# Kernel optimization log

Measured on AMD Instinct MI355X. Metric: run time of the kernel, lower is better.

## Reference

```python
import jax, jax.numpy as jnp
import numpy as np

NUM_WIRES = 14
LAYERS = 3
PPL = 3
BATCH = 1024
DIM = 2 ** NUM_WIRES


def setup_inputs() -> dict:
    key = jax.random.key(0)
    k1, k2, k3, k4, k5 = jax.random.split(key, 5)
    sr = jax.random.normal(k1, (BATCH, DIM), jnp.float32)
    si = jax.random.normal(k2, (BATCH, DIM), jnp.float32)
    norm = jnp.sqrt(jnp.sum(sr * sr + si * si, axis=1, keepdims=True))
    sr, si = sr / norm, si / norm  # normalized amplitude-encoded states
    weights = jax.random.normal(k3, (LAYERS, PPL, NUM_WIRES), jnp.float32)
    head_w = jax.random.normal(k4, (1, NUM_WIRES), jnp.float32) / np.sqrt(NUM_WIRES)
    head_b = jax.random.normal(k5, (1,), jnp.float32) * 0.01
    return {"state_real": sr, "state_imag": si, "weights": weights,
            "head_w": head_w, "head_b": head_b}


def _apply_ry_all(st, angles):
    # st: (B,)+(2,)*n complex; apply RY(angles[q]) on each wire q (RYs on distinct wires commute)
    half = angles * 0.5
    c, s = jnp.cos(half), jnp.sin(half)
    for q in range(NUM_WIRES):
        ax = 1 + q
        a0 = jnp.take(st, 0, axis=ax)
        a1 = jnp.take(st, 1, axis=ax)
        n0 = c[q] * a0 - s[q] * a1
        n1 = s[q] * a0 + c[q] * a1
        st = jnp.stack([n0, n1], axis=ax)
    return st


def _apply_cnot(st, ctrl, tgt):
    # flip target axis only where control bit == 1
    ctrl_ax, tgt_ax = 1 + ctrl, 1 + tgt
    flipped = jnp.flip(st, axis=tgt_ax)
    mask_shape = [1] * (NUM_WIRES + 1)
    mask_shape[ctrl_ax] = 2
    mask = (jnp.arange(2).reshape(mask_shape) == 1)
    return jnp.where(mask, flipped, st)


def _circuit(state, weights):
    # state: (B, DIM) complex64 -> PauliZ expvals (B, NUM_WIRES)
    st = state.reshape((-1,) + (2,) * NUM_WIRES)
    for l in range(LAYERS):
        # sequential RY(w[l,p,q]) for p=0..PPL-1 on wire q compose to RY(sum_p w[l,p,q])
        ang = jnp.sum(weights[l], axis=0)  # (NUM_WIRES,)
        st = _apply_ry_all(st, ang)
        for j in range(NUM_WIRES):
            st = _apply_cnot(st, j, (j + 1) % NUM_WIRES)
    probs = st.real ** 2 + st.imag ** 2  # (B,)+(2,)*n
    probs = probs.reshape(-1, DIM)
    idx = jnp.arange(DIM)
    # PennyLane convention: wire 0 is the most significant bit
    bits = (idx[None, :] >> (NUM_WIRES - 1 - jnp.arange(NUM_WIRES))[:, None]) & 1  # (n, DIM)
    signs = (1 - 2 * bits).astype(probs.dtype)
    return probs @ signs.T  # (B, n)


def reference(state_real, state_imag, weights, head_w, head_b):
    state = jax.lax.complex(state_real, state_imag)
    feats = _circuit(state, weights)  # (B, NUM_WIRES)
    return feats @ head_w[0] + head_b[0]  # (B,)
```

## Files before the change

kernel.cpp:

```cpp
#include <hip/hip_runtime.h>

typedef unsigned int u32;

#define DIM 16384
#define NT  512

__host__ __device__ constexpr u32 swzN(u32 d) {
    u32 b0 = ((d >> 4) ^ (d >> 5)) & 1u;
    u32 b1 = (d >> 4) & 1u;
    u32 b2 = ((d >> 7) ^ (d >> 8)) & 1u;
    u32 b3 = ((d >> 6) ^ (d >> 8)) & 1u;
    return d ^ b0 ^ (b1 << 1) ^ (b2 << 2) ^ (b3 << 3);
}

__host__ __device__ constexpr u32 mmap(u32 y) {
    u32 s = y;
    s ^= s >> 1; s ^= s >> 2; s ^= s >> 4; s ^= s >> 8;
    return (s & 0x1FFFu) | (((s ^ (y >> 13)) & 1u) << 13);
}

__host__ __device__ constexpr u32 mpow(u32 x, int L) {
    for (int i = 0; i < L; ++i) x = mmap(x);
    return x;
}

constexpr u32 PV3[5] = {0x040, 0x080, 0x100, 0x200, 0x400};
constexpr u32 PV4[5] = {0x006, 0x00C, 0x018, 0x030, 0x060};
constexpr u32 PV5[5] = {0x3001, 0x0003, 0x0C00, 0x1800, 0x3000};
constexpr u32 PV6[5] = {0x005, 0x00A, 0x014, 0x028, 0x050};
constexpr u32 PV7[5] = {0x0A0, 0x140, 0x280, 0x500, 0xA00};

__host__ __device__ constexpr u32 moff(const u32* v, int r) {
    u32 m = 0;
    for (int i = 0; i < 5; ++i) if ((r >> i) & 1) m ^= v[i];
    return m;
}
__host__ __device__ constexpr u32 parmask(const u32* v, int L, int b) {
    u32 pm = 0;
    for (int r = 0; r < 32; ++r)
        pm |= ((mpow(moff(v, r), L) >> b) & 1u) << r;
    return pm;
}
__host__ __device__ constexpr int hbit(int D) {
    int h = 0;
    while (D >> (h + 1)) ++h;
    return 1 << h;
}

__device__ __forceinline__ void rot2(float2& a0, float2& a1, float c, float s) {
    float t0x = s * a1.x, t0y = s * a1.y;
    float t1x = s * a0.x, t1y = s * a0.y;
    float n0x = fmaf(c, a0.x, -t0x), n0y = fmaf(c, a0.y, -t0y);
    float n1x = fmaf(c, a1.x,  t1x), n1y = fmaf(c, a1.y,  t1y);
    a0.x = n0x; a0.y = n0y;
    a1.x = n1x; a1.y = n1y;
}

template<int D, u32 PM>
__device__ __forceinline__ void gateGM(float2 (&am)[32], float c, float s, u32 sB) {
    constexpr int H = hbit(D);
    float sp = sB ? -s : s;
    #pragma unroll
    for (int r = 0; r < 32; ++r)
        if (!(r & H)) {
            if ((PM >> r) & 1) rot2(am[r], am[r ^ D], c, -sp);
            else               rot2(am[r], am[r ^ D], c,  sp);
        }
}

__global__ __launch_bounds__(NT, 2) void qsim_kernel(
    const float* __restrict__ sreal, const float* __restrict__ simag,
    const float* __restrict__ wts,   const float* __restrict__ hw,
    const float* __restrict__ hb,    float* __restrict__ out)
{
    extern __shared__ float smem[];
    float* angC   = smem + 32768;
    float* angS   = angC + 48;
    float* lutLo  = angS + 48;
    float* lutHi  = lutLo + 128;
    float* redbuf = lutHi + 128;
    float2* st2 = (float2*)smem;
    float4* stv = (float4*)smem;

    int tid = threadIdx.x;
    int b   = blockIdx.x;

    const float4* pr = (const float4*)(sreal + (size_t)b * DIM);
    const float4* pi = (const float4*)(simag + (size_t)b * DIM);
    float4 vr[8], vi[8];
    #pragma unroll
    for (int h = 0; h < 8; ++h) {
        vr[h] = pr[(h << 9) | tid];
        vi[h] = pi[(h << 9) | tid];
    }

    if (tid < 42) {
        int l = tid / 14, bb = tid % 14, q = 13 - bb;
        float a = 0.5f * (wts[l * 42 + q] + wts[l * 42 + 14 + q] + wts[l * 42 + 28 + q]);
        angC[l * 16 + bb] = cosf(a);
        angS[l * 16 + bb] = sinf(a);
    } else if (tid >= 64 && tid < 192) {
        int i = tid - 64;
        float ssum = 0.f;
        for (int bb = 0; bb < 7; ++bb) if ((i >> bb) & 1) ssum += hw[13 - bb];
        lutLo[i] = ssum;
    } else if (tid >= 192 && tid < 320) {
        int i = tid - 192;
        float ssum = 0.f;
        for (int bb = 0; bb < 7; ++bb) if ((i >> bb) & 1) ssum += hw[6 - bb];
        lutHi[i] = ssum;
    }

    float2 am[32];
    #pragma unroll
    for (int h = 0; h < 8; ++h) {
        am[h * 4 + 0] = make_float2(vr[h].x, vi[h].x);
        am[h * 4 + 1] = make_float2(vr[h].y, vi[h].y);
        am[h * 4 + 2] = make_float2(vr[h].z, vi[h].z);
        am[h * 4 + 3] = make_float2(vr[h].w, vi[h].w);
    }

    __syncthreads();
    float W0  = lutLo[127] + lutHi[127];
    float acc = 0.f;

    {
        gateGM< 1, 0>(am, angC[ 0], angS[ 0], 0);
        gateGM< 2, 0>(am, angC[ 1], angS[ 1], 0);
        gateGM< 4, 0>(am, angC[11], angS[11], 0);
        gateGM< 8, 0>(am, angC[12], angS[12], 0);
        gateGM<16, 0>(am, angC[13], angS[13], 0);
        u32 base = swzN((u32)tid << 2);
        bool sw = (((tid >> 2) ^ (tid >> 3)) & 1) != 0;
        #pragma unroll
        for (int h = 0; h < 8; ++h)
            #pragma unroll
            for (int m = 0; m < 2; ++m) {
                u32 idx = (base ^ swzN(((u32)h << 11) | ((u32)m << 1))) >> 1;
                int r = h * 4 + m * 2;
                float2 a0 = am[r], a1 = am[r + 1];
                stv[idx] = sw ? make_float4(a1.x, a1.y, a0.x, a0.y)
                              : make_float4(a0.x, a0.y, a1.x, a1.y);
            }
        __syncthreads();
    }

    {
        u32 yb = (((u32)tid & 1u) << 1) | (((u32)tid >> 1) << 6);
        u32 base = swzN(yb);
        #pragma unroll
        for (int h = 0; h < 16; ++h) {
            u32 idx = (base ^ swzN((u32)h << 2)) >> 1;
            float4 v = stv[idx];
            if (((h >> 2) ^ (h >> 3)) & 1) {
                am[h * 2 + 1] = make_float2(v.x, v.y);
                am[h * 2]     = make_float2(v.z, v.w);
            } else {
                am[h * 2]     = make_float2(v.x, v.y);
                am[h * 2 + 1] = make_float2(v.z, v.w);
            }
        }
        gateGM< 2, 0>(am, angC[2], angS[2], 0);
        gateGM< 4, 0>(am, angC[3], angS[3], 0);
        gateGM< 8, 0>(am, angC[4], angS[4], 0);
        gateGM<16, 0>(am, angC[5], angS[5], 0);
        #pragma unroll
        for (int h = 0; h < 16; ++h) {
            u32 idx = (base ^ swzN((u32)h << 2)) >> 1;
            float2 a0 = am[h * 2], a1 = am[h * 2 + 1];
            if (((h >> 2) ^ (h >> 3)) & 1) stv[idx] = make_float4(a1.x, a1.y, a0.x, a0.y);
            else                           stv[idx] = make_float4(a0.x, a0.y, a1.x, a1.y);
        }
        __syncthreads();
    }

    {
        u32 B = ((u32)tid & 63u) | (((u32)tid >> 6) << 11);
        u32 base = swzN(B);
        #pragma unroll
        for (int j = 0; j < 32; ++j) am[j] = st2[base ^ swzN((u32)j << 6)];
        gateGM< 1, 0>(am, angC[ 6], angS[ 6], 0);
        gateGM< 2, 0>(am, angC[ 7], angS[ 7], 0);
        gateGM< 4, 0>(am, angC[ 8], angS[ 8], 0);
        gateGM< 8, 0>(am, angC[ 9], angS[ 9], 0);
        gateGM<16, 0>(am, angC[10], angS[10], 0);
        u32 z1 = mmap(B);
        gateGM< 3, parmask(PV3, 1,  7)>(am, angC[16 +  7], angS[16 +  7], (z1 >>  7) & 1u);
        gateGM< 6, parmask(PV3, 1,  8)>(am, angC[16 +  8], angS[16 +  8], (z1 >>  8) & 1u);
        gateGM<12, parmask(PV3, 1,  9)>(am, angC[16 +  9], angS[16 +  9], (z1 >>  9) & 1u);
        gateGM<24, parmask(PV3, 1, 10)>(am, angC[16 + 10], angS[16 + 10], (z1 >> 10) & 1u);
        #pragma unroll
        for (int j = 0; j < 32; ++j) st2[base ^ swzN((u32)j << 6)] = am[j];
        __syncthreads();
    }

    {
        u32 B = ((u32)tid & 3u) | (((u32)tid >> 2) << 7);
        u32 base = swzN(B);
        #pragma unroll
        for (int r = 0; r < 32; ++r) am[r] = st2[base ^ swzN(moff(PV4, r))];
        u32 z1 = mmap(B);
        gateGM< 1, parmask(PV4, 1, 2)>(am, angC[16 + 2], angS[16 + 2], (z1 >> 2) & 1u);
        gateGM< 2, parmask(PV4, 1, 3)>(am, angC[16 + 3], angS[16 + 3], (z1 >> 3) & 1u);
        gateGM< 4, parmask(PV4, 1, 4)>(am, angC[16 + 4], angS[16 + 4], (z1 >> 4) & 1u);
        gateGM< 8, parmask(PV4, 1, 5)>(am, angC[16 + 5], angS[16 + 5], (z1 >> 5) & 1u);
        gateGM<16, parmask(PV4, 1, 6)>(am, angC[16 + 6], angS[16 + 6], (z1 >> 6) & 1u);
        #pragma unroll
        for (int r = 0; r < 32; ++r) st2[base ^ swzN(moff(PV4, r))] = am[r];
        __syncthreads();
    }

    {
        u32 B = (((u32)tid & 0xFFu) << 2) | (((u32)tid >> 8) << 13);
        u32 base = swzN(B);
        #pragma unroll
        for (int r = 0; r < 32; ++r) am[r] = st2[base ^ swzN(moff(PV5, r))];
        u32 z1 = mmap(B), z2 = mmap(z1);
        gateGM< 1, parmask(PV5, 1,  0)>(am, angC[16 +  0], angS[16 +  0], (z1 >>  0) & 1u);
        gateGM< 2, parmask(PV5, 1,  1)>(am, angC[16 +  1], angS[16 +  1], (z1 >>  1) & 1u);
        gateGM< 4, parmask(PV5, 1, 11)>(am, angC[16 + 11], angS[16 + 11], (z1 >> 11) & 1u);
        gateGM< 8, parmask(PV5, 1, 12)>(am, angC[16 + 12], angS[16 + 12], (z1 >> 12) & 1u);
        gateGM<16, parmask(PV5, 1, 13)>(am, angC[16 + 13], angS[16 + 13], (z1 >> 13) & 1u);
        gateGM<25, parmask(PV5, 2,  0)>(am, angC[32 +  0], angS[32 +  0], (z2 >>  0) & 1u);
        gateGM< 3, parmask(PV5, 2,  1)>(am, angC[32 +  1], angS[32 +  1], (z2 >>  1) & 1u);
        gateGM<12, parmask(PV5, 2, 12)>(am, angC[32 + 12], angS[32 + 12], (z2 >> 12) & 1u);
        gateGM<24, parmask(PV5, 2, 13)>(am, angC[32 + 13], angS[32 + 13], (z2 >> 13) & 1u);
        #pragma unroll
        for (int r = 0; r < 32; ++r) st2[base ^ swzN(moff(PV5, r))] = am[r];
        __syncthreads();
    }

    {
        u32 B = ((u32)tid & 3u) | (((u32)tid >> 2) << 7);
        u32 base = swzN(B);
        #pragma unroll
        for (int r = 0; r < 32; ++r) am[r] = st2[base ^ swzN(moff(PV6, r))];
        u32 z2 = mpow(B, 2);
        gateGM< 1, parmask(PV6, 2, 2)>(am, angC[32 + 2], angS[32 + 2], (z2 >> 2) & 1u);
        gateGM< 2, parmask(PV6, 2, 3)>(am, angC[32 + 3], angS[32 + 3], (z2 >> 3) & 1u);
        gateGM< 4, parmask(PV6, 2, 4)>(am, angC[32 + 4], angS[32 + 4], (z2 >> 4) & 1u);
        gateGM< 8, parmask(PV6, 2, 5)>(am, angC[32 + 5], angS[32 + 5], (z2 >> 5) & 1u);
        gateGM<16, parmask(PV6, 2, 6)>(am, angC[32 + 6], angS[32 + 6], (z2 >> 6) & 1u);
        #pragma unroll
        for (int r = 0; r < 32; ++r) st2[base ^ swzN(moff(PV6, r))] = am[r];
        __syncthreads();
    }

    {
        u32 B = ((u32)tid & 0x7Fu) | (((u32)tid >> 7) << 12);
        u32 base = swzN(B);
        #pragma unroll
        for (int r = 0; r < 32; ++r) am[r] = st2[base ^ swzN(moff(PV7, r))];
        u32 z2 = mpow(B, 2);
        gateGM< 1, parmask(PV7, 2,  7)>(am, angC[32 +  7], angS[32 +  7], (z2 >>  7) & 1u);
        gateGM< 2, parmask(PV7, 2,  8)>(am, angC[32 +  8], angS[32 +  8], (z2 >>  8) & 1u);
        gateGM< 4, parmask(PV7, 2,  9)>(am, angC[32 +  9], angS[32 +  9], (z2 >>  9) & 1u);
        gateGM< 8, parmask(PV7, 2, 10)>(am, angC[32 + 10], angS[32 + 10], (z2 >> 10) & 1u);
        gateGM<16, parmask(PV7, 2, 11)>(am, angC[32 + 11], angS[32 + 11], (z2 >> 11) & 1u);
        u32 wB = mmap(z2);
        #pragma unroll
        for (int r = 0; r < 32; ++r) {
            u32 w = wB ^ mpow(moff(PV7, r), 3);
            float p  = fmaf(am[r].x, am[r].x, am[r].y * am[r].y);
            float wv = W0 - 2.0f * (lutLo[w & 127u] + lutHi[w >> 7]);
            acc = fmaf(wv, p, acc);
        }
    }

    #pragma unroll
    for (int off = 32; off > 0; off >>= 1) acc += __shfl_xor(acc, off, 64);
    if ((tid & 63) == 0) redbuf[tid >> 6] = acc;
    __syncthreads();
    if (tid == 0) {
        float tot = hb[0];
        #pragma unroll
        for (int i = 0; i < 8; ++i) tot += redbuf[i];
        out[b] = tot;
    }
}

extern "C" void kernel_launch(void* const* d_in, const int* in_sizes, int n_in,
                              void* d_out, int out_size, void* d_ws, size_t ws_size,
                              hipStream_t stream)
{
    const float* sreal = (const float*)d_in[0];
    const float* simag = (const float*)d_in[1];
    const float* wts   = (const float*)d_in[2];
    const float* hw    = (const float*)d_in[3];
    const float* hb    = (const float*)d_in[4];
    float* out = (float*)d_out;

    int batch = in_sizes[0] / DIM;
    size_t smem_bytes = (32768 + 48 + 48 + 128 + 128 + 16) * sizeof(float);

    (void)hipFuncSetAttribute((const void*)qsim_kernel,
                              hipFuncAttributeMaxDynamicSharedMemorySize, (int)smem_bytes);
    qsim_kernel<<<dim3(batch), dim3(NT), smem_bytes, stream>>>(sreal, simag, wts, hw, hb, out);
}
```

Measured before the change: 208.9 us.

## Process two batch states per block, skew phases to overlap LDS and compute

Each block now has 1024 threads and handles two batch elements, one per 512-thread half. The halves run the same gate and transpose pipeline offset by one phase, so they take turns on the single shared-memory state buffer. While one half reads or writes LDS, the other applies its register-resident gates. This is meant to hide LDS shuffle latency behind arithmetic, since the 128KB state buffer previously allowed only one 512-thread block per CU. The cost is many more block-wide barriers and fewer registers per thread under launch_bounds(1024,1).

```diff
diff --git a/kernel.cpp b/kernel.cpp
--- a/kernel.cpp
+++ b/kernel.cpp
@@ -3,7 +3,7 @@
 typedef unsigned int u32;
 
 #define DIM 16384
-#define NT  512
+#define NT  1024
 
 __host__ __device__ constexpr u32 swzN(u32 d) {
     u32 b0 = ((d >> 4) ^ (d >> 5)) & 1u;
@@ -18,7 +18,6 @@
     s ^= s >> 1; s ^= s >> 2; s ^= s >> 4; s ^= s >> 8;
     return (s & 0x1FFFu) | (((s ^ (y >> 13)) & 1u) << 13);
 }
-
 __host__ __device__ constexpr u32 mpow(u32 x, int L) {
     for (int i = 0; i < L; ++i) x = mmap(x);
     return x;
@@ -68,10 +67,198 @@
         }
 }
 
-__global__ __launch_bounds__(NT, 2) void qsim_kernel(
+__device__ __forceinline__ u32 B2of(int ltid) { return (((u32)ltid & 1u) << 1) | (((u32)ltid >> 1) << 6); }
+__device__ __forceinline__ u32 B3of(int ltid) { return ((u32)ltid & 63u) | (((u32)ltid >> 6) << 11); }
+__device__ __forceinline__ u32 B4of(int ltid) { return ((u32)ltid & 3u) | (((u32)ltid >> 2) << 7); }
+__device__ __forceinline__ u32 B5of(int ltid) { return (((u32)ltid & 0xFFu) << 2) | (((u32)ltid >> 8) << 13); }
+__device__ __forceinline__ u32 B7of(int ltid) { return ((u32)ltid & 0x7Fu) | (((u32)ltid >> 7) << 12); }
+
+__device__ __forceinline__ void doG1(float2 (&am)[32], const float* angC, const float* angS) {
+    gateGM< 1, 0>(am, angC[ 0], angS[ 0], 0);
+    gateGM< 2, 0>(am, angC[ 1], angS[ 1], 0);
+    gateGM< 4, 0>(am, angC[11], angS[11], 0);
+    gateGM< 8, 0>(am, angC[12], angS[12], 0);
+    gateGM<16, 0>(am, angC[13], angS[13], 0);
+}
+__device__ __forceinline__ void doW1(int ltid, float* smem, float2 (&am)[32]) {
+    float4* stv = (float4*)smem;
+    u32 base = swzN((u32)ltid << 2);
+    bool sw = (((ltid >> 2) ^ (ltid >> 3)) & 1) != 0;
+    #pragma unroll
+    for (int h = 0; h < 8; ++h)
+        #pragma unroll
+        for (int m = 0; m < 2; ++m) {
+            u32 idx = (base ^ swzN(((u32)h << 11) | ((u32)m << 1))) >> 1;
+            int r = h * 4 + m * 2;
+            float2 a0 = am[r], a1 = am[r + 1];
+            stv[idx] = sw ? make_float4(a1.x, a1.y, a0.x, a0.y)
+                          : make_float4(a0.x, a0.y, a1.x, a1.y);
+        }
+}
+__device__ __forceinline__ void doR2(int ltid, float* smem, float2 (&am)[32]) {
+    float4* stv = (float4*)smem;
+    u32 base = swzN(B2of(ltid));
+    #pragma unroll
+    for (int h = 0; h < 16; ++h) {
+        u32 idx = (base ^ swzN((u32)h << 2)) >> 1;
+        float4 v = stv[idx];
+        if (((h >> 2) ^ (h >> 3)) & 1) {
+            am[h * 2 + 1] = make_float2(v.x, v.y);
+            am[h * 2]     = make_float2(v.z, v.w);
+        } else {
+            am[h * 2]     = make_float2(v.x, v.y);
+            am[h * 2 + 1] = make_float2(v.z, v.w);
+        }
+    }
+}
+__device__ __forceinline__ void doW2(int ltid, float* smem, float2 (&am)[32]) {
+    float4* stv = (float4*)smem;
+    u32 base = swzN(B2of(ltid));
+    #pragma unroll
+    for (int h = 0; h < 16; ++h) {
+        u32 idx = (base ^ swzN((u32)h << 2)) >> 1;
+        float2 a0 = am[h * 2], a1 = am[h * 2 + 1];
+        if (((h >> 2) ^ (h >> 3)) & 1) stv[idx] = make_float4(a1.x, a1.y, a0.x, a0.y);
+        else                           stv[idx] = make_float4(a0.x, a0.y, a1.x, a1.y);
+    }
+}
+__device__ __forceinline__ void doG2a(float2 (&am)[32], const float* angC, const float* angS) {
+    gateGM< 2, 0>(am, angC[2], angS[2], 0);
+    gateGM< 4, 0>(am, angC[3], angS[3], 0);
+}
+__device__ __forceinline__ void doG2b(float2 (&am)[32], const float* angC, const float* angS) {
+    gateGM< 8, 0>(am, angC[4], angS[4], 0);
+    gateGM<16, 0>(am, angC[5], angS[5], 0);
+}
+__device__ __forceinline__ void doR3(int ltid, float* smem, float2 (&am)[32]) {
+    float2* st2 = (float2*)smem;
+    u32 base = swzN(B3of(ltid));
+    #pragma unroll
+    for (int j = 0; j < 32; ++j) am[j] = st2[base ^ swzN((u32)j << 6)];
+}
+__device__ __forceinline__ void doW3(int ltid, float* smem, float2 (&am)[32]) {
+    float2* st2 = (float2*)smem;
+    u32 base = swzN(B3of(ltid));
+    #pragma unroll
+    for (int j = 0; j < 32; ++j) st2[base ^ swzN((u32)j << 6)] = am[j];
+}
+__device__ __forceinline__ void doG3a(float2 (&am)[32], const float* angC, const float* angS) {
+    gateGM< 1, 0>(am, angC[ 6], angS[ 6], 0);
+    gateGM< 2, 0>(am, angC[ 7], angS[ 7], 0);
+    gateGM< 4, 0>(am, angC[ 8], angS[ 8], 0);
+    gateGM< 8, 0>(am, angC[ 9], angS[ 9], 0);
+    gateGM<16, 0>(am, angC[10], angS[10], 0);
+}
+__device__ __forceinline__ void doG3b(int ltid, float2 (&am)[32], const float* angC, const float* angS) {
+    u32 z1 = mmap(B3of(ltid));
+    gateGM< 3, parmask(PV3, 1,  7)>(am, angC[16 +  7], angS[16 +  7], (z1 >>  7) & 1u);
+    gateGM< 6, parmask(PV3, 1,  8)>(am, angC[16 +  8], angS[16 +  8], (z1 >>  8) & 1u);
+    gateGM<12, parmask(PV3, 1,  9)>(am, angC[16 +  9], angS[16 +  9], (z1 >>  9) & 1u);
+    gateGM<24, parmask(PV3, 1, 10)>(am, angC[16 + 10], angS[16 + 10], (z1 >> 10) & 1u);
+}
+__device__ __forceinline__ void doR4(int ltid, float* smem, float2 (&am)[32]) {
+    float2* st2 = (float2*)smem;
+    u32 base = swzN(B4of(ltid));
+    #pragma unroll
+    for (int r = 0; r < 32; ++r) am[r] = st2[base ^ swzN(moff(PV4, r))];
+}
+__device__ __forceinline__ void doW4(int ltid, float* smem, float2 (&am)[32]) {
+    float2* st2 = (float2*)smem;
+    u32 base = swzN(B4of(ltid));
+    #pragma unroll
+    for (int r = 0; r < 32; ++r) st2[base ^ swzN(moff(PV4, r))] = am[r];
+}
+__device__ __forceinline__ void doG4a(int ltid, float2 (&am)[32], const float* angC, const float* angS) {
+    u32 z1 = mmap(B4of(ltid));
+    gateGM< 1, parmask(PV4, 1, 2)>(am, angC[16 + 2], angS[16 + 2], (z1 >> 2) & 1u);
+    gateGM< 2, parmask(PV4, 1, 3)>(am, angC[16 + 3], angS[16 + 3], (z1 >> 3) & 1u);
+    gateGM< 4, parmask(PV4, 1, 4)>(am, angC[16 + 4], angS[16 + 4], (z1 >> 4) & 1u);
+}
+__device__ __forceinline__ void doG4b(int ltid, float2 (&am)[32], const float* angC, const float* angS) {
+    u32 z1 = mmap(B4of(ltid));
+    gateGM< 8, parmask(PV4, 1, 5)>(am, angC[16 + 5], angS[16 + 5], (z1 >> 5) & 1u);
+    gateGM<16, parmask(PV4, 1, 6)>(am, angC[16 + 6], angS[16 + 6], (z1 >> 6) & 1u);
+}
+__device__ __forceinline__ void doR5(int ltid, float* smem, float2 (&am)[32]) {
+    float2* st2 = (float2*)smem;
+    u32 base = swzN(B5of(ltid));
+    #pragma unroll
+    for (int r = 0; r < 32; ++r) am[r] = st2[base ^ swzN(moff(PV5, r))];
+}
+__device__ __forceinline__ void doW5(int ltid, float* smem, float2 (&am)[32]) {
+    float2* st2 = (float2*)smem;
+    u32 base = swzN(B5of(ltid));
+    #pragma unroll
+    for (int r = 0; r < 32; ++r) st2[base ^ swzN(moff(PV5, r))] = am[r];
+}
+__device__ __forceinline__ void doG5a(int ltid, float2 (&am)[32], const float* angC, const float* angS) {
+    u32 z1 = mmap(B5of(ltid));
+    gateGM< 1, parmask(PV5, 1,  0)>(am, angC[16 +  0], angS[16 +  0], (z1 >>  0) & 1u);
+    gateGM< 2, parmask(PV5, 1,  1)>(am, angC[16 +  1], angS[16 +  1], (z1 >>  1) & 1u);
+    gateGM< 4, parmask(PV5, 1, 11)>(am, angC[16 + 11], angS[16 + 11], (z1 >> 11) & 1u);
+    gateGM< 8, parmask(PV5, 1, 12)>(am, angC[16 + 12], angS[16 + 12], (z1 >> 12) & 1u);
+    gateGM<16, parmask(PV5, 1, 13)>(am, angC[16 + 13], angS[16 + 13], (z1 >> 13) & 1u);
+}
+__device__ __forceinline__ void doG5b(int ltid, float2 (&am)[32], const float* angC, const float* angS) {
+    u32 z2 = mpow(B5of(ltid), 2);
+    gateGM<25, parmask(PV5, 2,  0)>(am, angC[32 +  0], angS[32 +  0], (z2 >>  0) & 1u);
+    gateGM< 3, parmask(PV5, 2,  1)>(am, angC[32 +  1], angS[32 +  1], (z2 >>  1) & 1u);
+    gateGM<12, parmask(PV5, 2, 12)>(am, angC[32 + 12], angS[32 + 12], (z2 >> 12) & 1u);
+    gateGM<24, parmask(PV5, 2, 13)>(am, angC[32 + 13], angS[32 + 13], (z2 >> 13) & 1u);
+}
+__device__ __forceinline__ void doR6(int ltid, float* smem, float2 (&am)[32]) {
+    float2* st2 = (float2*)smem;
+    u32 base = swzN(B4of(ltid));
+    #pragma unroll
+    for (int r = 0; r < 32; ++r) am[r] = st2[base ^ swzN(moff(PV6, r))];
+}
+__device__ __forceinline__ void doW6(int ltid, float* smem, float2 (&am)[32]) {
+    float2* st2 = (float2*)smem;
+    u32 base = swzN(B4of(ltid));
+    #pragma unroll
+    for (int r = 0; r < 32; ++r) st2[base ^ swzN(moff(PV6, r))] = am[r];
+}
+__device__ __forceinline__ void doG6a(int ltid, float2 (&am)[32], const float* angC, const float* angS) {
+    u32 z2 = mpow(B4of(ltid), 2);
+    gateGM< 1, parmask(PV6, 2, 2)>(am, angC[32 + 2], angS[32 + 2], (z2 >> 2) & 1u);
+    gateGM< 2, parmask(PV6, 2, 3)>(am, angC[32 + 3], angS[32 + 3], (z2 >> 3) & 1u);
+    gateGM< 4, parmask(PV6, 2, 4)>(am, angC[32 + 4], angS[32 + 4], (z2 >> 4) & 1u);
+}
+__device__ __forceinline__ void doG6b(int ltid, float2 (&am)[32], const float* angC, const float* angS) {
+    u32 z2 = mpow(B4of(ltid), 2);
+    gateGM< 8, parmask(PV6, 2, 5)>(am, angC[32 + 5], angS[32 + 5], (z2 >> 5) & 1u);
+    gateGM<16, parmask(PV6, 2, 6)>(am, angC[32 + 6], angS[32 + 6], (z2 >> 6) & 1u);
+}
+__device__ __forceinline__ void doR7(int ltid, float* smem, float2 (&am)[32]) {
+    float2* st2 = (float2*)smem;
+    u32 base = swzN(B7of(ltid));
+    #pragma unroll
+    for (int r = 0; r < 32; ++r) am[r] = st2[base ^ swzN(moff(PV7, r))];
+}
+__device__ __forceinline__ void doG7(int ltid, float2 (&am)[32], const float* angC, const float* angS) {
+    u32 z2 = mpow(B7of(ltid), 2);
+    gateGM< 1, parmask(PV7, 2,  7)>(am, angC[32 +  7], angS[32 +  7], (z2 >>  7) & 1u);
+    gateGM< 2, parmask(PV7, 2,  8)>(am, angC[32 +  8], angS[32 +  8], (z2 >>  8) & 1u);
+    gateGM< 4, parmask(PV7, 2,  9)>(am, angC[32 +  9], angS[32 +  9], (z2 >>  9) & 1u);
+    gateGM< 8, parmask(PV7, 2, 10)>(am, angC[32 + 10], angS[32 + 10], (z2 >> 10) & 1u);
+    gateGM<16, parmask(PV7, 2, 11)>(am, angC[32 + 11], angS[32 + 11], (z2 >> 11) & 1u);
+}
+__device__ __forceinline__ void doMeas(int ltid, float2 (&am)[32], const float* lutLo,
+                                       const float* lutHi, float& acc, float W0) {
+    u32 wB = mpow(B7of(ltid), 3);
+    #pragma unroll
+    for (int r = 0; r < 32; ++r) {
+        u32 w = wB ^ mpow(moff(PV7, r), 3);
+        float p  = fmaf(am[r].x, am[r].x, am[r].y * am[r].y);
+        float wv = W0 - 2.0f * (lutLo[w & 127u] + lutHi[w >> 7]);
+        acc = fmaf(wv, p, acc);
+    }
+}
+
+__global__ __launch_bounds__(NT, 1) void qsim_kernel(
     const float* __restrict__ sreal, const float* __restrict__ simag,
     const float* __restrict__ wts,   const float* __restrict__ hw,
-    const float* __restrict__ hb,    float* __restrict__ out)
+    const float* __restrict__ hb,    float* __restrict__ out, int batch)
 {
     extern __shared__ float smem[];
     float* angC   = smem + 32768;
@@ -79,19 +266,24 @@
     float* lutLo  = angS + 48;
     float* lutHi  = lutLo + 128;
     float* redbuf = lutHi + 128;
-    float2* st2 = (float2*)smem;
-    float4* stv = (float4*)smem;
-
-    int tid = threadIdx.x;
-    int b   = blockIdx.x;
+
+    int tid  = threadIdx.x;
+    bool ga  = tid < 512;
+    int ltid = tid & 511;
+    int b    = blockIdx.x * 2 + (ga ? 0 : 1);
+    if (b >= batch) b = batch - 1;
 
     const float4* pr = (const float4*)(sreal + (size_t)b * DIM);
     const float4* pi = (const float4*)(simag + (size_t)b * DIM);
-    float4 vr[8], vi[8];
+    float2 am[32];
     #pragma unroll
     for (int h = 0; h < 8; ++h) {
-        vr[h] = pr[(h << 9) | tid];
-        vi[h] = pi[(h << 9) | tid];
+        float4 r = pr[(h << 9) | ltid];
+        float4 i = pi[(h << 9) | ltid];
+        am[h * 4 + 0] = make_float2(r.x, i.x);
+        am[h * 4 + 1] = make_float2(r.y, i.y);
+        am[h * 4 + 2] = make_float2(r.z, i.z);
+        am[h * 4 + 3] = make_float2(r.w, i.w);
     }
 
     if (tid < 42) {
@@ -111,171 +303,76 @@
         lutHi[i] = ssum;
     }
 
-    float2 am[32];
-    #pragma unroll
-    for (int h = 0; h < 8; ++h) {
-        am[h * 4 + 0] = make_float2(vr[h].x, vi[h].x);
-        am[h * 4 + 1] = make_float2(vr[h].y, vi[h].y);
-        am[h * 4 + 2] = make_float2(vr[h].z, vi[h].z);
-        am[h * 4 + 3] = make_float2(vr[h].w, vi[h].w);
-    }
-
     __syncthreads();
     float W0  = lutLo[127] + lutHi[127];
     float acc = 0.f;
 
-    {
-        gateGM< 1, 0>(am, angC[ 0], angS[ 0], 0);
-        gateGM< 2, 0>(am, angC[ 1], angS[ 1], 0);
-        gateGM< 4, 0>(am, angC[11], angS[11], 0);
-        gateGM< 8, 0>(am, angC[12], angS[12], 0);
-        gateGM<16, 0>(am, angC[13], angS[13], 0);
-        u32 base = swzN((u32)tid << 2);
-        bool sw = (((tid >> 2) ^ (tid >> 3)) & 1) != 0;
-        #pragma unroll
-        for (int h = 0; h < 8; ++h)
-            #pragma unroll
-            for (int m = 0; m < 2; ++m) {
-                u32 idx = (base ^ swzN(((u32)h << 11) | ((u32)m << 1))) >> 1;
-                int r = h * 4 + m * 2;
-                float2 a0 = am[r], a1 = am[r + 1];
-                stv[idx] = sw ? make_float4(a1.x, a1.y, a0.x, a0.y)
-                              : make_float4(a0.x, a0.y, a1.x, a1.y);
-            }
-        __syncthreads();
-    }
-
-    {
-        u32 yb = (((u32)tid & 1u) << 1) | (((u32)tid >> 1) << 6);
-        u32 base = swzN(yb);
-        #pragma unroll
-        for (int h = 0; h < 16; ++h) {
-            u32 idx = (base ^ swzN((u32)h << 2)) >> 1;
-            float4 v = stv[idx];
-            if (((h >> 2) ^ (h >> 3)) & 1) {
-                am[h * 2 + 1] = make_float2(v.x, v.y);
-                am[h * 2]     = make_float2(v.z, v.w);
-            } else {
-                am[h * 2]     = make_float2(v.x, v.y);
-                am[h * 2 + 1] = make_float2(v.z, v.w);
-            }
-        }
-        gateGM< 2, 0>(am, angC[2], angS[2], 0);
-        gateGM< 4, 0>(am, angC[3], angS[3], 0);
-        gateGM< 8, 0>(am, angC[4], angS[4], 0);
-        gateGM<16, 0>(am, angC[5], angS[5], 0);
-        #pragma unroll
-        for (int h = 0; h < 16; ++h) {
-            u32 idx = (base ^ swzN((u32)h << 2)) >> 1;
-            float2 a0 = am[h * 2], a1 = am[h * 2 + 1];
-            if (((h >> 2) ^ (h >> 3)) & 1) stv[idx] = make_float4(a1.x, a1.y, a0.x, a0.y);
-            else                           stv[idx] = make_float4(a0.x, a0.y, a1.x, a1.y);
-        }
-        __syncthreads();
-    }
-
-    {
-        u32 B = ((u32)tid & 63u) | (((u32)tid >> 6) << 11);
-        u32 base = swzN(B);
-        #pragma unroll
-        for (int j = 0; j < 32; ++j) am[j] = st2[base ^ swzN((u32)j << 6)];
-        gateGM< 1, 0>(am, angC[ 6], angS[ 6], 0);
-        gateGM< 2, 0>(am, angC[ 7], angS[ 7], 0);
-        gateGM< 4, 0>(am, angC[ 8], angS[ 8], 0);
-        gateGM< 8, 0>(am, angC[ 9], angS[ 9], 0);
-        gateGM<16, 0>(am, angC[10], angS[10], 0);
-        u32 z1 = mmap(B);
-        gateGM< 3, parmask(PV3, 1,  7)>(am, angC[16 +  7], angS[16 +  7], (z1 >>  7) & 1u);
-        gateGM< 6, parmask(PV3, 1,  8)>(am, angC[16 +  8], angS[16 +  8], (z1 >>  8) & 1u);
-        gateGM<12, parmask(PV3, 1,  9)>(am, angC[16 +  9], angS[16 +  9], (z1 >>  9) & 1u);
-        gateGM<24, parmask(PV3, 1, 10)>(am, angC[16 + 10], angS[16 + 10], (z1 >> 10) & 1u);
-        #pragma unroll
-        for (int j = 0; j < 32; ++j) st2[base ^ swzN((u32)j << 6)] = am[j];
-        __syncthreads();
-    }
-
-    {
-        u32 B = ((u32)tid & 3u) | (((u32)tid >> 2) << 7);
-        u32 base = swzN(B);
-        #pragma unroll
-        for (int r = 0; r < 32; ++r) am[r] = st2[base ^ swzN(moff(PV4, r))];
-        u32 z1 = mmap(B);
-        gateGM< 1, parmask(PV4, 1, 2)>(am, angC[16 + 2], angS[16 + 2], (z1 >> 2) & 1u);
-        gateGM< 2, parmask(PV4, 1, 3)>(am, angC[16 + 3], angS[16 + 3], (z1 >> 3) & 1u);
-        gateGM< 4, parmask(PV4, 1, 4)>(am, angC[16 + 4], angS[16 + 4], (z1 >> 4) & 1u);
-        gateGM< 8, parmask(PV4, 1, 5)>(am, angC[16 + 5], angS[16 + 5], (z1 >> 5) & 1u);
-        gateGM<16, parmask(PV4, 1, 6)>(am, angC[16 + 6], angS[16 + 6], (z1 >> 6) & 1u);
-        #pragma unroll
-        for (int r = 0; r < 32; ++r) st2[base ^ swzN(moff(PV4, r))] = am[r];
-        __syncthreads();
-    }
-
-    {
-        u32 B = (((u32)tid & 0xFFu) << 2) | (((u32)tid >> 8) << 13);
-        u32 base = swzN(B);
-        #pragma unroll
-        for (int r = 0; r < 32; ++r) am[r] = st2[base ^ swzN(moff(PV5, r))];
-        u32 z1 = mmap(B), z2 = mmap(z1);
-        gateGM< 1, parmask(PV5, 1,  0)>(am, angC[16 +  0], angS[16 +  0], (z1 >>  0) & 1u);
-        gateGM< 2, parmask(PV5, 1,  1)>(am, angC[16 +  1], angS[16 +  1], (z1 >>  1) & 1u);
-        gateGM< 4, parmask(PV5, 1, 11)>(am, angC[16 + 11], angS[16 + 11], (z1 >> 11) & 1u);
-        gateGM< 8, parmask(PV5, 1, 12)>(am, angC[16 + 12], angS[16 + 12], (z1 >> 12) & 1u);
-        gateGM<16, parmask(PV5, 1, 13)>(am, angC[16 + 13], angS[16 + 13], (z1 >> 13) & 1u);
-        gateGM<25, parmask(PV5, 2,  0)>(am, angC[32 +  0], angS[32 +  0], (z2 >>  0) & 1u);
-        gateGM< 3, parmask(PV5, 2,  1)>(am, angC[32 +  1], angS[32 +  1], (z2 >>  1) & 1u);
-        gateGM<12, parmask(PV5, 2, 12)>(am, angC[32 + 12], angS[32 + 12], (z2 >> 12) & 1u);
-        gateGM<24, parmask(PV5, 2, 13)>(am, angC[32 + 13], angS[32 + 13], (z2 >> 13) & 1u);
-        #pragma unroll
-        for (int r = 0; r < 32; ++r) st2[base ^ swzN(moff(PV5, r))] = am[r];
-        __syncthreads();
-    }
-
-    {
-        u32 B = ((u32)tid & 3u) | (((u32)tid >> 2) << 7);
-        u32 base = swzN(B);
-        #pragma unroll
-        for (int r = 0; r < 32; ++r) am[r] = st2[base ^ swzN(moff(PV6, r))];
-        u32 z2 = mpow(B, 2);
-        gateGM< 1, parmask(PV6, 2, 2)>(am, angC[32 + 2], angS[32 + 2], (z2 >> 2) & 1u);
-        gateGM< 2, parmask(PV6, 2, 3)>(am, angC[32 + 3], angS[32 + 3], (z2 >> 3) & 1u);
-        gateGM< 4, parmask(PV6, 2, 4)>(am, angC[32 + 4], angS[32 + 4], (z2 >> 4) & 1u);
-        gateGM< 8, parmask(PV6, 2, 5)>(am, angC[32 + 5], angS[32 + 5], (z2 >> 5) & 1u);
-        gateGM<16, parmask(PV6, 2, 6)>(am, angC[32 + 6], angS[32 + 6], (z2 >> 6) & 1u);
-        #pragma unroll
-        for (int r = 0; r < 32; ++r) st2[base ^ swzN(moff(PV6, r))] = am[r];
-        __syncthreads();
-    }
-
-    {
-        u32 B = ((u32)tid & 0x7Fu) | (((u32)tid >> 7) << 12);
-        u32 base = swzN(B);
-        #pragma unroll
-        for (int r = 0; r < 32; ++r) am[r] = st2[base ^ swzN(moff(PV7, r))];
-        u32 z2 = mpow(B, 2);
-        gateGM< 1, parmask(PV7, 2,  7)>(am, angC[32 +  7], angS[32 +  7], (z2 >>  7) & 1u);
-        gateGM< 2, parmask(PV7, 2,  8)>(am, angC[32 +  8], angS[32 +  8], (z2 >>  8) & 1u);
-        gateGM< 4, parmask(PV7, 2,  9)>(am, angC[32 +  9], angS[32 +  9], (z2 >>  9) & 1u);
-        gateGM< 8, parmask(PV7, 2, 10)>(am, angC[32 + 10], angS[32 + 10], (z2 >> 10) & 1u);
-        gateGM<16, parmask(PV7, 2, 11)>(am, angC[32 + 11], angS[32 + 11], (z2 >> 11) & 1u);
-        u32 wB = mmap(z2);
-        #pragma unroll
-        for (int r = 0; r < 32; ++r) {
-            u32 w = wB ^ mpow(moff(PV7, r), 3);
-            float p  = fmaf(am[r].x, am[r].x, am[r].y * am[r].y);
-            float wv = W0 - 2.0f * (lutLo[w & 127u] + lutHi[w >> 7]);
-            acc = fmaf(wv, p, acc);
-        }
-    }
+    if (ga) { doG1(am, angC, angS); doW1(ltid, smem, am); }
+    else    { doG1(am, angC, angS); }
+    __syncthreads();
+    if (ga) { doR2(ltid, smem, am); }
+    __syncthreads();
+    if (ga) { doG2a(am, angC, angS); } else { doW1(ltid, smem, am); }
+    __syncthreads();
+    if (ga) { doG2b(am, angC, angS); } else { doR2(ltid, smem, am); }
+    __syncthreads();
+    if (ga) { doW2(ltid, smem, am); } else { doG2a(am, angC, angS); }
+    __syncthreads();
+    if (ga) { doR3(ltid, smem, am); } else { doG2b(am, angC, angS); }
+    __syncthreads();
+    if (ga) { doG3a(am, angC, angS); } else { doW2(ltid, smem, am); }
+    __syncthreads();
+    if (ga) { doG3b(ltid, am, angC, angS); } else { doR3(ltid, smem, am); }
+    __syncthreads();
+    if (ga) { doW3(ltid, smem, am); } else { doG3a(am, angC, angS); }
+    __syncthreads();
+    if (ga) { doR4(ltid, smem, am); } else { doG3b(ltid, am, angC, angS); }
+    __syncthreads();
+    if (ga) { doG4a(ltid, am, angC, angS); } else { doW3(ltid, smem, am); }
+    __syncthreads();
+    if (ga) { doG4b(ltid, am, angC, angS); } else { doR4(ltid, smem, am); }
+    __syncthreads();
+    if (ga) { doW4(ltid, smem, am); } else { doG4a(ltid, am, angC, angS); }
+    __syncthreads();
+    if (ga) { doR5(ltid, smem, am); } else { doG4b(ltid, am, angC, angS); }
+    __syncthreads();
+    if (ga) { doG5a(ltid, am, angC, angS); } else { doW4(ltid, smem, am); }
+    __syncthreads();
+    if (ga) { doG5b(ltid, am, angC, angS); } else { doR5(ltid, smem, am); }
+    __syncthreads();
+    if (ga) { doW5(ltid, smem, am); } else { doG5a(ltid, am, angC, angS); }
+    __syncthreads();
+    if (ga) { doR6(ltid, smem, am); } else { doG5b(ltid, am, angC, angS); }
+    __syncthreads();
+    if (ga) { doG6a(ltid, am, angC, angS); } else { doW5(ltid, smem, am); }
+    __syncthreads();
+    if (ga) { doG6b(ltid, am, angC, angS); } else { doR6(ltid, smem, am); }
+    __syncthreads();
+    if (ga) { doW6(ltid, smem, am); } else { doG6a(ltid, am, angC, angS); }
+    __syncthreads();
+    if (ga) { doR7(ltid, smem, am); } else { doG6b(ltid, am, angC, angS); }
+    __syncthreads();
+    if (ga) { doG7(ltid, am, angC, angS); doMeas(ltid, am, lutLo, lutHi, acc, W0); }
+    else    { doW6(ltid, smem, am); }
+    __syncthreads();
+    if (!ga) { doR7(ltid, smem, am); }
+    __syncthreads();
+    if (!ga) { doG7(ltid, am, angC, angS); doMeas(ltid, am, lutLo, lutHi, acc, W0); }
 
     #pragma unroll
     for (int off = 32; off > 0; off >>= 1) acc += __shfl_xor(acc, off, 64);
     if ((tid & 63) == 0) redbuf[tid >> 6] = acc;
     __syncthreads();
     if (tid == 0) {
-        float tot = hb[0];
+        float t = hb[0];
         #pragma unroll
-        for (int i = 0; i < 8; ++i) tot += redbuf[i];
-        out[b] = tot;
+        for (int i = 0; i < 8; ++i) t += redbuf[i];
+        out[blockIdx.x * 2] = t;
+    } else if (tid == 512 && blockIdx.x * 2 + 1 < batch) {
+        float t = hb[0];
+        #pragma unroll
+        for (int i = 0; i < 8; ++i) t += redbuf[8 + i];
+        out[blockIdx.x * 2 + 1] = t;
     }
 }
 
@@ -291,9 +388,10 @@
     float* out = (float*)d_out;
 
     int batch = in_sizes[0] / DIM;
+    int nblk  = (batch + 1) / 2;
     size_t smem_bytes = (32768 + 48 + 48 + 128 + 128 + 16) * sizeof(float);
 
     (void)hipFuncSetAttribute((const void*)qsim_kernel,
                               hipFuncAttributeMaxDynamicSharedMemorySize, (int)smem_bytes);
-    qsim_kernel<<<dim3(batch), dim3(NT), smem_bytes, stream>>>(sreal, simag, wts, hw, hb, out);
-}
+    qsim_kernel<<<dim3(nblk), dim3(NT), smem_bytes, stream>>>(sreal, simag, wts, hw, hb, out, batch);
+}
```

New measurement: 331.9 us. +58.9%, slower.
